# Kernel optimization log

Measured on AMD Instinct MI355X. Metric: run time of the kernel, lower is better.

The kernel has to match this reference:

```python
import jax, jax.numpy as jnp
import numpy as np

B, L, DIM, ET, NH, SD, NC = 32, 200, 36, 128, 64, 9, 2


def setup_inputs() -> dict:
    key = jax.random.key(0)
    ks = jax.random.split(key, 16)
    f = jnp.float32
    vals = jax.random.normal(ks[0], (B, L, DIM), f)
    obs = (jax.random.uniform(ks[1], (B, L, DIM)) < 0.7).astype(f)  # 0/1 observation mask
    x = jnp.concatenate([vals, obs], -1)                            # (B, L, 2*DIM)
    time_steps = jnp.sort(jax.random.uniform(ks[2], (B, L)), axis=1)
    static_info = jax.random.normal(ks[3], (B, SD), f)
    query_param = jnp.linspace(0.0, 1.0, ET, dtype=f)               # nn.Parameter(linspace)

    def lin(k, o, i, s):
        return jax.random.normal(k, (o, i), f) * s

    return dict(
        x=x, time_steps=time_steps, static_info=static_info, query_param=query_param,
        periodic_w=lin(ks[4], ET - 1, 1, 1.0), periodic_b=jnp.zeros((ET - 1,), f),
        timelin_w=lin(ks[5], 1, 1, 1.0), timelin_b=jnp.zeros((1,), f),
        qw=lin(ks[6], ET, ET, ET ** -0.5), qb=jnp.zeros((ET,), f),
        kw=lin(ks[7], ET, ET, ET ** -0.5), kb=jnp.zeros((ET,), f),
        ow=lin(ks[8], DIM, 2 * DIM, (2 * DIM) ** -0.5), ob=jnp.zeros((DIM,), f),
        gru_w_ih=lin(ks[9], 3 * NH, DIM, DIM ** -0.5),
        gru_w_hh=lin(ks[10], 3 * NH, NH, NH ** -0.5),
        gru_b_ih=jnp.zeros((3 * NH,), f), gru_b_hh=jnp.zeros((3 * NH,), f),
        st_w=lin(ks[11], 8, SD, SD ** -0.5), st_b=jnp.zeros((8,), f),
        c1_w=lin(ks[12], NH + 8, NH + 8, (NH + 8) ** -0.5), c1_b=jnp.zeros((NH + 8,), f),
        bn_g=jnp.ones((NH + 8,), f), bn_b=jnp.zeros((NH + 8,), f),
        c2_w=lin(ks[13], NC, NH + 8, (NH + 8) ** -0.5), c2_b=jnp.zeros((NC,), f),
        rand_mask=jax.random.randint(ks[14], (B, L), 0, 2, jnp.int32),
    )


def reference(x, time_steps, static_info, query_param, periodic_w, periodic_b,
              timelin_w, timelin_b, qw, qb, kw, kb, ow, ob,
              gru_w_ih, gru_w_hh, gru_b_ih, gru_b_hh, st_w, st_b,
              c1_w, c1_b, bn_g, bn_b, c2_w, c2_b, rand_mask):
    dim = x.shape[-1] // 2
    irr = x[:, :, dim:]                                   # observation mask channels
    temp = rand_mask.astype(x.dtype)[:, :, None]          # random_masking keep-mask
    m_small = irr * temp
    irr2 = jnp.concatenate([irr, irr], -1)                # (B, L, 2*dim)
    m2 = jnp.concatenate([m_small, m_small], -1)

    def time_emb(tt):
        tt = tt[..., None]
        return jnp.concatenate([tt @ timelin_w.T + timelin_b,
                                jnp.sin(tt @ periodic_w.T + periodic_b)], -1)

    key_e = time_emb(time_steps)                          # (B, L, ET)
    query_e = time_emb(query_param[None, :])[0]           # (ET, ET)
    q = query_e @ qw.T + qb                               # num_heads=1 => dk=ET
    k = key_e @ kw.T + kb
    scores = jnp.einsum('qd,bld->bql', q, k) / jnp.sqrt(jnp.asarray(ET, x.dtype))

    def mta(mask):
        # per-channel masked softmax over keys l: (B, Lq, L, 2*dim)
        s5 = jnp.where(mask[:, None, :, :] == 0, jnp.asarray(-1e9, x.dtype),
                       scores[:, :, :, None])
        p = jax.nn.softmax(s5, axis=2)
        o = jnp.einsum('bqld,bld->bqd', p, x)             # (B, Lq, 2*dim)
        return o @ ow.T + ob                              # (B, Lq, dim)

    out_te = mta(irr2)
    out1_te = mta(m2)

    sx = x[:, :, :dim]
    sx_g = jnp.round(jax.nn.sigmoid(jnp.einsum('bld,ble->bde', sx, sx)))
    sout = jax.nn.sigmoid(jnp.einsum('bqd,bqe->bde', out_te, out_te))

    def step(h, xt):  # torch GRU cell, gate order r,z,n
        gi = xt @ gru_w_ih.T + gru_b_ih
        gh = h @ gru_w_hh.T + gru_b_hh
        ir, iz, inn = jnp.split(gi, 3, -1)
        hr, hz, hn = jnp.split(gh, 3, -1)
        r = jax.nn.sigmoid(ir + hr)
        z = jax.nn.sigmoid(iz + hz)
        n = jnp.tanh(inn + r * hn)
        return (1 - z) * n + z * h, None

    h0 = jnp.zeros((x.shape[0], gru_w_hh.shape[1]), x.dtype)
    h_fin, _ = jax.lax.scan(step, h0, jnp.swapaxes(out_te, 0, 1))

    st = static_info @ st_w.T + st_b
    cls_in = jnp.concatenate([h_fin, st], 1)
    z1 = cls_in @ c1_w.T + c1_b
    mu = z1.mean(0)
    var = z1.var(0)                                       # BatchNorm1d (training stats)
    zn = (z1 - mu) / jnp.sqrt(var + 1e-5) * bn_g + bn_b
    zg = jax.nn.gelu(zn, approximate=False)
    logits = zg @ c2_w.T + c2_b
    return (out_te, out1_te, logits, sx_g, sout, query_param)
```

## Files before the change

### kernel.cpp

```cpp
#include <hip/hip_runtime.h>

#define B_   32
#define L_   200
#define DIM_ 36
#define ET_  128
#define NH_  64
#define SD_  9
#define NC_  2

#define O_TE   0
#define O_T1   147456
#define O_LG   294912
#define O_SXG  294976
#define O_SOUT 336448
#define O_QP   377920

typedef __fp16 half_t;
typedef __attribute__((ext_vector_type(2))) __fp16 half2_t;

__device__ __forceinline__ float sigm(float x) { return 1.f / (1.f + expf(-x)); }
__device__ __forceinline__ float fsigm(float x) {
  return __builtin_amdgcn_rcpf(1.f + __expf(-x));
}
__device__ __forceinline__ float ftanh(float x) {
  return 2.f * __builtin_amdgcn_rcpf(1.f + __expf(-2.f * x)) - 1.f;
}
__device__ __forceinline__ half2_t f2h2(float a, float b) {
  return __builtin_amdgcn_cvt_pkrtz(a, b);
}
__device__ __forceinline__ float dot2acc(half2_t w, half2_t h, float acc) {
#if __has_builtin(__builtin_amdgcn_fdot2)
  return __builtin_amdgcn_fdot2(w, h, acc, false);
#else
  return acc + (float)w.x * (float)h.x + (float)w.y * (float)h.y;
#endif
}

__global__ __launch_bounds__(256) void k_pre2(
    const float* __restrict__ qw, const float* __restrict__ kw,
    const float* __restrict__ qb, const float* __restrict__ qp,
    const float* __restrict__ pw, const float* __restrict__ pb,
    const float* __restrict__ tlw, const float* __restrict__ tlb,
    const float* __restrict__ ts, const float* __restrict__ x,
    const int* __restrict__ rm,
    float* __restrict__ qm2, float* __restrict__ xmean,
    float* __restrict__ ks_ws, half2_t* __restrict__ w_ws,
    float* __restrict__ out) {
  int blk = blockIdx.x, t = threadIdx.x;
  if (blk < 128) {
    __shared__ float eq[128];
    __shared__ float uq[128];
    int q = blk;
    if (t < 128) {
      float tt = qp[q];
      eq[t] = (t == 0) ? tt * tlw[0] + tlb[0]
                       : __sinf(tt * pw[t - 1] + pb[t - 1]);
    }
    __syncthreads();
    if (t < 128) {
      const float4* qw4 = (const float4*)(qw + (size_t)t * 128);
      float a = qb[t];
      #pragma unroll 8
      for (int c = 0; c < 32; c++) {
        float4 w = qw4[c];
        a += eq[4 * c] * w.x + eq[4 * c + 1] * w.y +
             eq[4 * c + 2] * w.z + eq[4 * c + 3] * w.w;
      }
      uq[t] = a;
    }
    __syncthreads();
    if (t < 128) {
      float a = 0.f;
      #pragma unroll 8
      for (int i = 0; i < 128; i++) a += uq[i] * kw[i * 128 + t];
      qm2[q * 128 + t] = a * 0.088388347648318447f;
      if (q == 0) out[O_QP + t] = qp[t];
    }
    return;
  }
  if (blk < 160) {
    int b = blk - 128;
    if (t < 72) {
      float s = 0.f;
      const float* xb = x + (size_t)b * L_ * 72 + t;
      #pragma unroll 8
      for (int l = 0; l < L_; l++) s += xb[(size_t)l * 72];
      xmean[b * 72 + t] = s * (1.0f / L_);
    }
    return;
  }
  if (blk < 224) {
    int bb = (blk - 160) >> 1, half = (blk - 160) & 1;
    float tl_w = tlw[0], tl_b = tlb[0];
    const float* tsb = ts + bb * L_;
    float* dst = ks_ws + (size_t)bb * 25600;
    for (int i = half * 12800 + t; i < half * 12800 + 12800; i += 256) {
      int l = i >> 7, j = i & 127;
      float tt = tsb[l];
      float e = (j == 0) ? tt * tl_w + tl_b
                         : __sinf(tt * pw[j - 1] + pb[j - 1]);
      int blkj = (j >> 2) ^ ((l >> 2) & 7);
      dst[(l << 7) + (blkj << 2) + (j & 3)] = e;
    }
    return;
  }
  {
    int bb = blk - 224;
    const float2* xb2 = (const float2*)(x + (size_t)bb * L_ * 72);
    const int* rmb = rm + bb * L_;
    half2_t* wd = w_ws + (size_t)bb * 14400;
    for (int i = t; i < L_ * 72; i += 256) {
      int l = i / 72, c2 = i % 72;
      int seg = c2 / 18, fh = c2 % 18;
      float2 v = xb2[l * 36 + fh];
      float2 o = xb2[l * 36 + 18 + fh];
      float rr = (float)rmb[l];
      float w0, w1;
      if (seg == 0)      { w0 = o.x * v.x;      w1 = o.y * v.y; }
      else if (seg == 1) { w0 = o.x;            w1 = o.y; }
      else if (seg == 2) { w0 = o.x * v.x * rr; w1 = o.y * v.y * rr; }
      else               { w0 = o.x * rr;       w1 = o.y * rr; }
      wd[l * 72 + c2] = f2h2(w0, w1);
    }
  }
}

__global__ __launch_bounds__(1024, 1) void k_attn(
    const float* __restrict__ qm, const float* __restrict__ ks_ws,
    const half2_t* __restrict__ w_ws,
    const float* __restrict__ xmean, const float* __restrict__ ow,
    const float* __restrict__ ob, float* __restrict__ out) {
  __shared__ __align__(16) char Abuf[103936];
  __shared__ __align__(16) float qs[16][128];
  __shared__ __align__(16) float sc[16][200];
  __shared__ __align__(16) float owsh[DIM_][72];
  float*   ksA  = (float*)Abuf;
  half2_t* wsh2 = (half2_t*)Abuf;
  float*   sums = (float*)(Abuf + 57600);
  float*   ofr  = (float*)(Abuf + 57600 + 36864);

  int b = blockIdx.x >> 3;
  int q0 = (blockIdx.x & 7) << 4;
  int tid = threadIdx.x;

  const float4* qsrc = (const float4*)(qm + q0 * ET_);
  for (int i = tid; i < 16 * 32; i += 1024) ((float4*)qs)[i] = qsrc[i];
  const float4* owsrc = (const float4*)ow;
  for (int i = tid; i < DIM_ * 18; i += 1024) ((float4*)owsh)[i] = owsrc[i];
  {
    const float4* kssrc = (const float4*)(ks_ws + (size_t)b * 25600);
    for (int i = tid; i < 6400; i += 1024) ((float4*)ksA)[i] = kssrc[i];
  }
  __syncthreads();

  {
    int w = tid >> 6, lg = tid & 63;
    int qp2 = w >> 1;
    int lh = w & 1;
    float acc[2][2];
    #pragma unroll
    for (int i = 0; i < 2; i++)
      #pragma unroll
      for (int j = 0; j < 2; j++) acc[i][j] = 0.f;
    const float4* ks4 = (const float4*)ksA;
    const float4* qs4 = (const float4*)qs;
    int lbase = 100 * lh + 2 * lg;
    int swz0 = (lbase >> 2) & 7;
    int swz1 = ((lbase + 1) >> 2) & 7;
    #pragma unroll 4
    for (int d4 = 0; d4 < 32; d4++) {
      float4 kv[2];
      {
        int l0c = (lbase < 100 * lh + 100) ? lbase : (100 * lh + 99);
        int l1c = (lbase + 1 < 100 * lh + 100) ? lbase + 1 : (100 * lh + 99);
        kv[0] = ks4[(l0c << 5) + (d4 ^ swz0)];
        kv[1] = ks4[(l1c << 5) + (d4 ^ swz1)];
      }
      #pragma unroll
      for (int i = 0; i < 2; i++) {
        float4 qv = qs4[(2 * qp2 + i) * 32 + d4];
        #pragma unroll
        for (int j = 0; j < 2; j++)
          acc[i][j] += qv.x * kv[j].x + qv.y * kv[j].y +
                       qv.z * kv[j].z + qv.w * kv[j].w;
      }
    }
    if (2 * lg < 100) {
      #pragma unroll
      for (int i = 0; i < 2; i++) {
        float2 v = {acc[i][0], acc[i][1]};
        *((float2*)(&sc[2 * qp2 + i][lbase])) = v;
      }
    }
  }
  __syncthreads();

  {
    int qi = tid >> 6, li = tid & 63;
    float m = -1e30f;
    for (int l = li; l < L_; l += 64) m = fmaxf(m, sc[qi][l]);
    #pragma unroll
    for (int off = 32; off >= 1; off >>= 1) m = fmaxf(m, __shfl_xor(m, off));
    for (int l = li; l < L_; l += 64) sc[qi][l] = __expf(sc[qi][l] - m);
  }

  {
    const float4* wsrc = (const float4*)(w_ws + (size_t)b * 14400);
    for (int i = tid; i < 3600; i += 1024) ((float4*)wsh2)[i] = wsrc[i];
  }
  __syncthreads();

  {
    int quarter = tid >> 8, tt = tid & 255;
    int qi = tt >> 4, li = tt & 15;
    int l0 = quarter * 50;
    float accA[8], accB[8];
    #pragma unroll
    for (int k = 0; k < 8; k++) { accA[k] = 0.f; accB[k] = 0.f; }
    const float4* wA = (const float4*)wsh2;
    #pragma unroll 2
    for (int l = l0; l < l0 + 50; l++) {
      float ev = sc[qi][l];
      float4 wa = wA[l * 18 + li];
      union { float f; half2_t h; } u0, u1, u2, u3;
      u0.f = wa.x; u1.f = wa.y; u2.f = wa.z; u3.f = wa.w;
      accA[0] += ev * (float)u0.h.x; accA[1] += ev * (float)u0.h.y;
      accA[2] += ev * (float)u1.h.x; accA[3] += ev * (float)u1.h.y;
      accA[4] += ev * (float)u2.h.x; accA[5] += ev * (float)u2.h.y;
      accA[6] += ev * (float)u3.h.x; accA[7] += ev * (float)u3.h.y;
      if (li < 2) {
        float4 wb = wA[l * 18 + 16 + li];
        union { float f; half2_t h; } b0, b1, b2, b3;
        b0.f = wb.x; b1.f = wb.y; b2.f = wb.z; b3.f = wb.w;
        accB[0] += ev * (float)b0.h.x; accB[1] += ev * (float)b0.h.y;
        accB[2] += ev * (float)b1.h.x; accB[3] += ev * (float)b1.h.y;
        accB[4] += ev * (float)b2.h.x; accB[5] += ev * (float)b2.h.y;
        accB[6] += ev * (float)b3.h.x; accB[7] += ev * (float)b3.h.y;
      }
    }
    float* sq = sums + quarter * 2304 + qi * 144;
    float4* sA = (float4*)(sq + 8 * li);
    sA[0] = make_float4(accA[0], accA[1], accA[2], accA[3]);
    sA[1] = make_float4(accA[4], accA[5], accA[6], accA[7]);
    if (li < 2) {
      float4* sB = (float4*)(sq + 128 + 8 * li);
      sB[0] = make_float4(accB[0], accB[1], accB[2], accB[3]);
      sB[1] = make_float4(accB[4], accB[5], accB[6], accB[7]);
    }
  }
  __syncthreads();

  const float* xm = xmean + b * 72;
  for (int idx = tid; idx < 16 * DIM_; idx += 1024) {
    int qq = idx / DIM_, j = idx % DIM_;
    const float* s0 = sums + qq * 144;
    const float* s1 = s0 + 2304;
    const float* s2 = s1 + 2304;
    const float* s3 = s2 + 2304;
    float numA = (s0[j] + s1[j]) + (s2[j] + s3[j]);
    float denA = (s0[36 + j] + s1[36 + j]) + (s2[36 + j] + s3[36 + j]);
    float numB = (s0[72 + j] + s1[72 + j]) + (s2[72 + j] + s3[72 + j]);
    float denB = (s0[108 + j] + s1[108 + j]) + (s2[108 + j] + s3[108 + j]);
    float al, ah, bl, bh;
    if (denA > 0.f) { al = numA / denA; ah = 1.f; }
    else            { al = xm[j];       ah = xm[36 + j]; }
    if (denB > 0.f) { bl = numB / denB; bh = 1.f; }
    else            { bl = xm[j];       bh = xm[36 + j]; }
    float* oq = ofr + qq * 144;
    oq[j] = al;      oq[36 + j] = ah;
    oq[72 + j] = bl; oq[108 + j] = bh;
  }
  __syncthreads();

  for (int idx = tid; idx < 16 * 72; idx += 1024) {
    int qq = idx / 72, t = idx % 72;
    int v = t / DIM_, i2 = t % DIM_;
    const float4* o4 = (const float4*)(ofr + qq * 144 + v * 72);
    const float4* w4 = (const float4*)(owsh[i2]);
    float a = ob[i2];
    #pragma unroll
    for (int d4 = 0; d4 < 18; d4++) {
      float4 ov = o4[d4], wv = w4[d4];
      a += ov.x * wv.x + ov.y * wv.y + ov.z * wv.z + ov.w * wv.w;
    }
    size_t off = ((size_t)b * ET_ + q0 + qq) * DIM_ + i2;
    out[(v == 0 ? O_TE : O_T1) + off] = a;
  }
}

__global__ __launch_bounds__(256, 1) void k_sg(
    const float* __restrict__ out_ro, const float* __restrict__ x,
    const float* __restrict__ wih, const float* __restrict__ bih,
    const float* __restrict__ whh, const float* __restrict__ bhh,
    const float* __restrict__ si, const float* __restrict__ stw,
    const float* __restrict__ stb, const float* __restrict__ c1w,
    const float* __restrict__ c1b, const float* __restrict__ bng,
    const float* __restrict__ bnb, const float* __restrict__ c2w,
    const float* __restrict__ c2b,
    float* __restrict__ hfin, int* __restrict__ ctr,
    float* __restrict__ out) {
  __shared__ __align__(16) float ote_s[ET_][DIM_];
  __shared__ float gis[ET_][3 * NH_];
  __shared__ __align__(16) half2_t hpk[NH_ / 2];
  int blk = blockIdx.x, t = threadIdx.x;

  if (blk >= 64) {
    float* base = &gis[0][0];
    float (*cin)[72] = (float(*)[72])(base);
    float (*z1)[72]  = (float(*)[72])(base + 2304);
    float (*zg)[72]  = (float(*)[72])(base + 4608);
    float* c1wt = base + 6912;
    float* c2ws = base + 6912 + 5184;
    float* bngs = c2ws + 144;
    float* bnbs = bngs + 72;
    for (int idx = t; idx < 72 * 72; idx += 256) {
      int j = idx / 72, d = idx % 72;
      c1wt[d * 72 + j] = c1w[idx];
    }
    for (int idx = t; idx < NC_ * 72; idx += 256) c2ws[idx] = c2w[idx];
    if (t < 72) { bngs[t] = bng[t]; bnbs[t] = bnb[t]; }
    for (int idx = t; idx < B_ * 8; idx += 256) {
      int b = idx / 8, j = idx % 8;
      float acc = stb[j];
      #pragma unroll
      for (int d = 0; d < SD_; d++) acc += si[b * SD_ + d] * stw[j * SD_ + d];
      cin[b][NH_ + j] = acc;
    }
    __syncthreads();
    if (t == 0) {
      while (__hip_atomic_load(ctr, __ATOMIC_ACQUIRE,
                               __HIP_MEMORY_SCOPE_AGENT) < 32)
        __builtin_amdgcn_s_sleep(8);
    }
    __syncthreads();
    for (int idx = t; idx < B_ * NH_; idx += 256)
      cin[idx / NH_][idx % NH_] = hfin[idx];
    __syncthreads();
    for (int idx = t; idx < B_ * 72; idx += 256) {
      int b = idx / 72, j = idx % 72;
      float acc = c1b[j];
      #pragma unroll 8
      for (int d = 0; d < 72; d++) acc += cin[b][d] * c1wt[d * 72 + j];
      z1[b][j] = acc;
    }
    __syncthreads();
    if (t < 72) {
      float mu = 0.f;
      for (int b = 0; b < B_; b++) mu += z1[b][t];
      mu *= (1.f / B_);
      float vv = 0.f;
      for (int b = 0; b < B_; b++) { float d = z1[b][t] - mu; vv += d * d; }
      vv *= (1.f / B_);
      float inv = 1.f / sqrtf(vv + 1e-5f);
      float g = bngs[t], bb = bnbs[t];
      for (int b = 0; b < B_; b++) {
        float zn = (z1[b][t] - mu) * inv * g + bb;
        zg[b][t] = 0.5f * zn * (1.f + erff(zn * 0.70710678118654752f));
      }
    }
    __syncthreads();
    for (int idx = t; idx < B_ * NC_; idx += 256) {
      int b = idx / NC_, c = idx % NC_;
      float acc = c2b[c];
      #pragma unroll 8
      for (int d = 0; d < 72; d++) acc += zg[b][d] * c2ws[c * 72 + d];
      out[O_LG + idx] = acc;
    }
    return;
  }

  if (blk < 32) {
    int b = blk;
    float* sxs = (float*)gis;
    const float4* osrc = (const float4*)(out_ro + O_TE + (size_t)b * ET_ * DIM_);
    for (int idx = t; idx < ET_ * 9; idx += 256)
      ((float4*)&ote_s[0][0])[idx] = osrc[idx];
    const float4* xsrc = (const float4*)(x + (size_t)b * L_ * 72);
    for (int idx = t; idx < L_ * 18; idx += 256) {
      int l = idx / 18, c = idx % 18;
      ((float4*)&sxs[l * 76])[c] = xsrc[idx];
    }
    __syncthreads();
    for (int idx = t; idx < DIM_ * DIM_; idx += 256) {
      int d = idx / DIM_, e = idx % DIM_;
      float s = 0.f;
      #pragma unroll 8
      for (int q = 0; q < ET_; q++) s += ote_s[q][d] * ote_s[q][e];
      out[O_SOUT + (size_t)b * DIM_ * DIM_ + idx] = sigm(s);
    }
    for (int idx = t; idx < DIM_ * DIM_; idx += 256) {
      int d = idx / DIM_, e = idx % DIM_;
      float s = 0.f;
      #pragma unroll 8
      for (int l = 0; l < L_; l++) s += sxs[l * 76 + d] * sxs[l * 76 + e];
      out[O_SXG + (size_t)b * DIM_ * DIM_ + idx] = rintf(sigm(s));
    }
    return;
  }

  int b = blk - 32;
  const float* ote = out_ro + O_TE;
  const float4* osrc = (const float4*)(ote + (size_t)b * ET_ * DIM_);
  for (int idx = t; idx < ET_ * DIM_ / 4; idx += 256)
    ((float4*)&ote_s[0][0])[idx] = osrc[idx];
  __syncthreads();

  if (t < 3 * NH_) {
    float wv[DIM_];
    const float* wrow = wih + (size_t)t * DIM_;
    #pragma unroll
    for (int d = 0; d < DIM_; d++) wv[d] = wrow[d];
    float bi = bih[t] + ((t < 2 * NH_) ? bhh[t] : 0.f);
    for (int q = 0; q < ET_; q++) {
      const float4* xr = (const float4*)ote_s[q];
      float a = bi;
      #pragma unroll
      for (int c = 0; c < 9; c++) {
        float4 xv = xr[c];
        a += xv.x * wv[4 * c] + xv.y * wv[4 * c + 1] +
             xv.z * wv[4 * c + 2] + xv.w * wv[4 * c + 3];
      }
      gis[q][t] = a;
    }
  }
  __syncthreads();
  if (t >= 64) return;

  half2_t wr[32], wz[32], wn[32];
  {
    const float2* r0 = (const float2*)(whh + (size_t)t * NH_);
    const float2* r1 = (const float2*)(whh + (size_t)(NH_ + t) * NH_);
    const float2* r2 = (const float2*)(whh + (size_t)(2 * NH_ + t) * NH_);
    #pragma unroll
    for (int c = 0; c < 32; c++) {
      float2 a = r0[c], bb = r1[c], cc = r2[c];
      wr[c] = f2h2(a.x, a.y);
      wz[c] = f2h2(bb.x, bb.y);
      wn[c] = f2h2(cc.x, cc.y);
    }
  }
  float bh_n = bhh[2 * NH_ + t];

  float h = 0.f;
  ((half_t*)hpk)[t] = (half_t)0.f;
  for (int q = 0; q < ET_; q++) {
    float gi_r = gis[q][t];
    float gi_z = gis[q][NH_ + t];
    float gi_n = gis[q][2 * NH_ + t];
    float ar = 0.f, az = 0.f, an = 0.f;
    const float4* hp4 = (const float4*)hpk;
    #pragma unroll
    for (int c4 = 0; c4 < 8; c4++) {
      float4 hv = hp4[c4];
      union { float f; half2_t h; } u0, u1, u2, u3;
      u0.f = hv.x; u1.f = hv.y; u2.f = hv.z; u3.f = hv.w;
      int c = c4 * 4;
      ar = dot2acc(wr[c + 0], u0.h, ar);
      az = dot2acc(wz[c + 0], u0.h, az);
      an = dot2acc(wn[c + 0], u0.h, an);
      ar = dot2acc(wr[c + 1], u1.h, ar);
      az = dot2acc(wz[c + 1], u1.h, az);
      an = dot2acc(wn[c + 1], u1.h, an);
      ar = dot2acc(wr[c + 2], u2.h, ar);
      az = dot2acc(wz[c + 2], u2.h, az);
      an = dot2acc(wn[c + 2], u2.h, an);
      ar = dot2acc(wr[c + 3], u3.h, ar);
      az = dot2acc(wz[c + 3], u3.h, az);
      an = dot2acc(wn[c + 3], u3.h, an);
    }
    float r = fsigm(gi_r + ar);
    float z = fsigm(gi_z + az);
    float n = ftanh(gi_n + r * (an + bh_n));
    h = n + z * (h - n);
    ((half_t*)hpk)[t] = (half_t)h;
  }
  hfin[b * NH_ + t] = h;
  __threadfence();
  if (t == 0) atomicAdd(ctr, 1);
}

extern "C" void kernel_launch(void* const* d_in, const int* in_sizes, int n_in,
                              void* d_out, int out_size, void* d_ws,
                              size_t ws_size, hipStream_t stream) {
  const float* x    = (const float*)d_in[0];
  const float* ts   = (const float*)d_in[1];
  const float* si   = (const float*)d_in[2];
  const float* qp   = (const float*)d_in[3];
  const float* pw   = (const float*)d_in[4];
  const float* pb   = (const float*)d_in[5];
  const float* tlw  = (const float*)d_in[6];
  const float* tlb  = (const float*)d_in[7];
  const float* qw   = (const float*)d_in[8];
  const float* qb   = (const float*)d_in[9];
  const float* kw   = (const float*)d_in[10];
  const float* ow   = (const float*)d_in[12];
  const float* ob   = (const float*)d_in[13];
  const float* wih  = (const float*)d_in[14];
  const float* whh  = (const float*)d_in[15];
  const float* bih  = (const float*)d_in[16];
  const float* bhh  = (const float*)d_in[17];
  const float* stw  = (const float*)d_in[18];
  const float* stb  = (const float*)d_in[19];
  const float* c1w  = (const float*)d_in[20];
  const float* c1b  = (const float*)d_in[21];
  const float* bng  = (const float*)d_in[22];
  const float* bnb  = (const float*)d_in[23];
  const float* c2w  = (const float*)d_in[24];
  const float* c2b  = (const float*)d_in[25];
  const int*   rm   = (const int*)d_in[26];

  float* out = (float*)d_out;

  float* W = (float*)d_ws;
  float*   ws_qm2   = W;
  float*   ws_xmean = W + 16384;
  float*   ws_hfin  = W + 18688;
  int*     ws_ctr   = (int*)(W + 20736);
  float*   ws_ks    = W + 20800;
  half2_t* ws_w     = (half2_t*)(W + 20800 + 819200);

  hipMemsetAsync(ws_ctr, 0, sizeof(int), stream);
  hipLaunchKernelGGL(k_pre2, dim3(256), dim3(256), 0, stream,
                     qw, kw, qb, qp, pw, pb, tlw, tlb, ts, x, rm,
                     ws_qm2, ws_xmean, ws_ks, ws_w, out);
  hipLaunchKernelGGL(k_attn, dim3(B_ * 8), dim3(1024), 0, stream,
                     ws_qm2, ws_ks, ws_w, ws_xmean, ow, ob, out);
  hipLaunchKernelGGL(k_sg, dim3(65), dim3(256), 0, stream,
                     out, x, wih, bih, whh, bhh, si, stw, stb, c1w, c1b,
                     bng, bnb, c2w, c2b, ws_hfin, ws_ctr, out);
}
```

Baseline: 226.4 us.

## Interleave two batch GRU recurrences per block to hide serial step latency

Each GRU block now processes two batch elements, running their hidden-state recurrences interleaved with separate accumulators so independent dot-product chains overlap. The second batch's input gates are spilled to a workspace buffer in global memory and prefetched one step ahead, since shared memory only holds one gate table. The grid shrinks from 65 to 49 blocks and the classifier waits on 16 completions. The risk is roughly doubled per-step instruction work on one wave, which can lengthen the serial chain if it was issue-bound rather than latency-bound.

```diff
diff --git a/kernel.cpp b/kernel.cpp
--- a/kernel.cpp
+++ b/kernel.cpp
@@ -298,13 +298,14 @@
     const float* __restrict__ bnb, const float* __restrict__ c2w,
     const float* __restrict__ c2b,
     float* __restrict__ hfin, int* __restrict__ ctr,
-    float* __restrict__ out) {
-  __shared__ __align__(16) float ote_s[ET_][DIM_];
+    float* __restrict__ gi1ws, float* __restrict__ out) {
+  __shared__ __align__(16) float ote_s[2][ET_][DIM_];
   __shared__ float gis[ET_][3 * NH_];
-  __shared__ __align__(16) half2_t hpk[NH_ / 2];
+  __shared__ __align__(16) half2_t hpk0[NH_ / 2];
+  __shared__ __align__(16) half2_t hpk1[NH_ / 2];
   int blk = blockIdx.x, t = threadIdx.x;
 
-  if (blk >= 64) {
+  if (blk >= 48) {
     float* base = &gis[0][0];
     float (*cin)[72] = (float(*)[72])(base);
     float (*z1)[72]  = (float(*)[72])(base + 2304);
@@ -329,7 +330,7 @@
     __syncthreads();
     if (t == 0) {
       while (__hip_atomic_load(ctr, __ATOMIC_ACQUIRE,
-                               __HIP_MEMORY_SCOPE_AGENT) < 32)
+                               __HIP_MEMORY_SCOPE_AGENT) < 16)
         __builtin_amdgcn_s_sleep(8);
     }
     __syncthreads();
@@ -374,7 +375,7 @@
     float* sxs = (float*)gis;
     const float4* osrc = (const float4*)(out_ro + O_TE + (size_t)b * ET_ * DIM_);
     for (int idx = t; idx < ET_ * 9; idx += 256)
-      ((float4*)&ote_s[0][0])[idx] = osrc[idx];
+      ((float4*)&ote_s[0][0][0])[idx] = osrc[idx];
     const float4* xsrc = (const float4*)(x + (size_t)b * L_ * 72);
     for (int idx = t; idx < L_ * 18; idx += 256) {
       int l = idx / 18, c = idx % 18;
@@ -385,7 +386,7 @@
       int d = idx / DIM_, e = idx % DIM_;
       float s = 0.f;
       #pragma unroll 8
-      for (int q = 0; q < ET_; q++) s += ote_s[q][d] * ote_s[q][e];
+      for (int q = 0; q < ET_; q++) s += ote_s[0][q][d] * ote_s[0][q][e];
       out[O_SOUT + (size_t)b * DIM_ * DIM_ + idx] = sigm(s);
     }
     for (int idx = t; idx < DIM_ * DIM_; idx += 256) {
@@ -398,12 +399,20 @@
     return;
   }
 
-  int b = blk - 32;
+  int ib = blk - 32;
+  int b0 = ib * 2, b1 = b0 + 1;
   const float* ote = out_ro + O_TE;
-  const float4* osrc = (const float4*)(ote + (size_t)b * ET_ * DIM_);
-  for (int idx = t; idx < ET_ * DIM_ / 4; idx += 256)
-    ((float4*)&ote_s[0][0])[idx] = osrc[idx];
-  __syncthreads();
+  {
+    const float4* o0 = (const float4*)(ote + (size_t)b0 * ET_ * DIM_);
+    const float4* o1 = (const float4*)(ote + (size_t)b1 * ET_ * DIM_);
+    for (int idx = t; idx < ET_ * 9; idx += 256) {
+      ((float4*)&ote_s[0][0][0])[idx] = o0[idx];
+      ((float4*)&ote_s[1][0][0])[idx] = o1[idx];
+    }
+  }
+  __syncthreads();
+
+  float* gi1 = gi1ws + (size_t)ib * ET_ * 192;
 
   if (t < 3 * NH_) {
     float wv[DIM_];
@@ -412,15 +421,19 @@
     for (int d = 0; d < DIM_; d++) wv[d] = wrow[d];
     float bi = bih[t] + ((t < 2 * NH_) ? bhh[t] : 0.f);
     for (int q = 0; q < ET_; q++) {
-      const float4* xr = (const float4*)ote_s[q];
-      float a = bi;
+      const float4* xr0 = (const float4*)ote_s[0][q];
+      const float4* xr1 = (const float4*)ote_s[1][q];
+      float a0 = bi, a1 = bi;
       #pragma unroll
       for (int c = 0; c < 9; c++) {
-        float4 xv = xr[c];
-        a += xv.x * wv[4 * c] + xv.y * wv[4 * c + 1] +
-             xv.z * wv[4 * c + 2] + xv.w * wv[4 * c + 3];
-      }
-      gis[q][t] = a;
+        float4 x0 = xr0[c], x1 = xr1[c];
+        a0 += x0.x * wv[4 * c] + x0.y * wv[4 * c + 1] +
+              x0.z * wv[4 * c + 2] + x0.w * wv[4 * c + 3];
+        a1 += x1.x * wv[4 * c] + x1.y * wv[4 * c + 1] +
+              x1.z * wv[4 * c + 2] + x1.w * wv[4 * c + 3];
+      }
+      gis[q][t] = a0;
+      gi1[q * 192 + t] = a1;
     }
   }
   __syncthreads();
@@ -441,40 +454,70 @@
   }
   float bh_n = bhh[2 * NH_ + t];
 
-  float h = 0.f;
-  ((half_t*)hpk)[t] = (half_t)0.f;
+  float h0 = 0.f, h1 = 0.f;
+  ((half_t*)hpk0)[t] = (half_t)0.f;
+  ((half_t*)hpk1)[t] = (half_t)0.f;
+  float gr1 = gi1[t], gz1 = gi1[NH_ + t], gn1 = gi1[2 * NH_ + t];
   for (int q = 0; q < ET_; q++) {
-    float gi_r = gis[q][t];
-    float gi_z = gis[q][NH_ + t];
-    float gi_n = gis[q][2 * NH_ + t];
-    float ar = 0.f, az = 0.f, an = 0.f;
-    const float4* hp4 = (const float4*)hpk;
+    float gr1n = 0.f, gz1n = 0.f, gn1n = 0.f;
+    if (q + 1 < ET_) {
+      const float* gp = gi1 + (q + 1) * 192;
+      gr1n = gp[t]; gz1n = gp[NH_ + t]; gn1n = gp[2 * NH_ + t];
+    }
+    float gr0 = gis[q][t];
+    float gz0 = gis[q][NH_ + t];
+    float gn0 = gis[q][2 * NH_ + t];
+    float ar0 = 0.f, az0 = 0.f, an0 = 0.f;
+    float ar1 = 0.f, az1 = 0.f, an1 = 0.f;
+    const float4* hp40 = (const float4*)hpk0;
+    const float4* hp41 = (const float4*)hpk1;
     #pragma unroll
     for (int c4 = 0; c4 < 8; c4++) {
-      float4 hv = hp4[c4];
-      union { float f; half2_t h; } u0, u1, u2, u3;
-      u0.f = hv.x; u1.f = hv.y; u2.f = hv.z; u3.f = hv.w;
+      float4 hv0 = hp40[c4];
+      float4 hv1 = hp41[c4];
+      union { float f; half2_t h; } a0, a1_, a2, a3, b0_, b1_, b2_, b3_;
+      a0.f = hv0.x; a1_.f = hv0.y; a2.f = hv0.z; a3.f = hv0.w;
+      b0_.f = hv1.x; b1_.f = hv1.y; b2_.f = hv1.z; b3_.f = hv1.w;
       int c = c4 * 4;
-      ar = dot2acc(wr[c + 0], u0.h, ar);
-      az = dot2acc(wz[c + 0], u0.h, az);
-      an = dot2acc(wn[c + 0], u0.h, an);
-      ar = dot2acc(wr[c + 1], u1.h, ar);
-      az = dot2acc(wz[c + 1], u1.h, az);
-      an = dot2acc(wn[c + 1], u1.h, an);
-      ar = dot2acc(wr[c + 2], u2.h, ar);
-      az = dot2acc(wz[c + 2], u2.h, az);
-      an = dot2acc(wn[c + 2], u2.h, an);
-      ar = dot2acc(wr[c + 3], u3.h, ar);
-      az = dot2acc(wz[c + 3], u3.h, az);
-      an = dot2acc(wn[c + 3], u3.h, an);
-    }
-    float r = fsigm(gi_r + ar);
-    float z = fsigm(gi_z + az);
-    float n = ftanh(gi_n + r * (an + bh_n));
-    h = n + z * (h - n);
-    ((half_t*)hpk)[t] = (half_t)h;
-  }
-  hfin[b * NH_ + t] = h;
+      ar0 = dot2acc(wr[c + 0], a0.h, ar0);
+      ar1 = dot2acc(wr[c + 0], b0_.h, ar1);
+      az0 = dot2acc(wz[c + 0], a0.h, az0);
+      az1 = dot2acc(wz[c + 0], b0_.h, az1);
+      an0 = dot2acc(wn[c + 0], a0.h, an0);
+      an1 = dot2acc(wn[c + 0], b0_.h, an1);
+      ar0 = dot2acc(wr[c + 1], a1_.h, ar0);
+      ar1 = dot2acc(wr[c + 1], b1_.h, ar1);
+      az0 = dot2acc(wz[c + 1], a1_.h, az0);
+      az1 = dot2acc(wz[c + 1], b1_.h, az1);
+      an0 = dot2acc(wn[c + 1], a1_.h, an0);
+      an1 = dot2acc(wn[c + 1], b1_.h, an1);
+      ar0 = dot2acc(wr[c + 2], a2.h, ar0);
+      ar1 = dot2acc(wr[c + 2], b2_.h, ar1);
+      az0 = dot2acc(wz[c + 2], a2.h, az0);
+      az1 = dot2acc(wz[c + 2], b2_.h, az1);
+      an0 = dot2acc(wn[c + 2], a2.h, an0);
+      an1 = dot2acc(wn[c + 2], b2_.h, an1);
+      ar0 = dot2acc(wr[c + 3], a3.h, ar0);
+      ar1 = dot2acc(wr[c + 3], b3_.h, ar1);
+      az0 = dot2acc(wz[c + 3], a3.h, az0);
+      az1 = dot2acc(wz[c + 3], b3_.h, az1);
+      an0 = dot2acc(wn[c + 3], a3.h, an0);
+      an1 = dot2acc(wn[c + 3], b3_.h, an1);
+    }
+    float r0 = fsigm(gr0 + ar0);
+    float r1 = fsigm(gr1 + ar1);
+    float z0 = fsigm(gz0 + az0);
+    float z1 = fsigm(gz1 + az1);
+    float n0 = ftanh(gn0 + r0 * (an0 + bh_n));
+    float n1 = ftanh(gn1 + r1 * (an1 + bh_n));
+    h0 = n0 + z0 * (h0 - n0);
+    h1 = n1 + z1 * (h1 - n1);
+    ((half_t*)hpk0)[t] = (half_t)h0;
+    ((half_t*)hpk1)[t] = (half_t)h1;
+    gr1 = gr1n; gz1 = gz1n; gn1 = gn1n;
+  }
+  hfin[b0 * NH_ + t] = h0;
+  hfin[b1 * NH_ + t] = h1;
   __threadfence();
   if (t == 0) atomicAdd(ctr, 1);
 }
@@ -518,6 +561,7 @@
   int*     ws_ctr   = (int*)(W + 20736);
   float*   ws_ks    = W + 20800;
   half2_t* ws_w     = (half2_t*)(W + 20800 + 819200);
+  float*   ws_gi1   = W + 20800 + 819200 + 460800;
 
   hipMemsetAsync(ws_ctr, 0, sizeof(int), stream);
   hipLaunchKernelGGL(k_pre2, dim3(256), dim3(256), 0, stream,
@@ -525,7 +569,7 @@
                      ws_qm2, ws_xmean, ws_ks, ws_w, out);
   hipLaunchKernelGGL(k_attn, dim3(B_ * 8), dim3(1024), 0, stream,
                      ws_qm2, ws_ks, ws_w, ws_xmean, ow, ob, out);
-  hipLaunchKernelGGL(k_sg, dim3(65), dim3(256), 0, stream,
+  hipLaunchKernelGGL(k_sg, dim3(49), dim3(256), 0, stream,
                      out, x, wih, bih, whh, bhh, si, stw, stb, c1w, c1b,
-                     bng, bnb, c2w, c2b, ws_hfin, ws_ctr, out);
-}
+                     bng, bnb, c2w, c2b, ws_hfin, ws_ctr, ws_gi1, out);
+}
```

New measurement: 304.9 us. 34.7% more time.
